# Kernel tuning notes

Measured on AMD Instinct MI355X. Metric: run time of the kernel, lower is better.

Reference implementation:

```python
import jax, jax.numpy as jnp
import numpy as np

N = 50000      # nodes
E = 800000     # edges (avg degree 16)
H = 128        # hidden_channels
L = 4          # num_layers
MAXZ = 100
EPS = 1e-5


def setup_inputs() -> dict:
    key = jax.random.key(0)
    ks = jax.random.split(key, 16)
    s = 0.05
    return {
        "z": jax.random.randint(ks[0], (N,), 0, MAXZ),
        "pos": jax.random.normal(ks[1], (N, 3), dtype=jnp.float32),
        "edge_index": jax.random.randint(ks[2], (2, E), 0, N),
        "emb": jax.random.normal(ks[3], (MAXZ, H), dtype=jnp.float32) * s,
        # edge_mlp: Linear(2H+1 -> H), SiLU, Linear(H -> H), SiLU
        "edge_w1": jax.random.normal(ks[4], (L, 2 * H + 1, H), dtype=jnp.float32) * s,
        "edge_b1": jnp.zeros((L, H), dtype=jnp.float32),
        "edge_w2": jax.random.normal(ks[5], (L, H, H), dtype=jnp.float32) * s,
        "edge_b2": jnp.zeros((L, H), dtype=jnp.float32),
        # node_mlp: Linear(2H -> H), SiLU, Linear(H -> H)
        "node_w1": jax.random.normal(ks[6], (L, 2 * H, H), dtype=jnp.float32) * s,
        "node_b1": jnp.zeros((L, H), dtype=jnp.float32),
        "node_w2": jax.random.normal(ks[7], (L, H, H), dtype=jnp.float32) * s,
        "node_b2": jnp.zeros((L, H), dtype=jnp.float32),
        "ln_g": jnp.ones((L, H), dtype=jnp.float32),
        "ln_b": jnp.zeros((L, H), dtype=jnp.float32),
    }


def _layernorm(x, g, b):
    mu = jnp.mean(x, axis=-1, keepdims=True)
    var = jnp.mean((x - mu) ** 2, axis=-1, keepdims=True)
    return g * (x - mu) / jnp.sqrt(var + EPS) + b


def reference(z, pos, edge_index, emb, edge_w1, edge_b1, edge_w2, edge_b2,
              node_w1, node_b1, node_w2, node_b2, ln_g, ln_b):
    row, col = edge_index[0], edge_index[1]
    # update_coords=False: pos is loop-invariant, so rel_pos/dist_sq computed once
    rel = pos[row] - pos[col]                       # [E, 3]
    d2 = jnp.sum(rel * rel, axis=-1, keepdims=True)  # [E, 1]
    h = emb[z]                                       # [N, H]
    n = h.shape[0]
    for l in range(L):
        edge_in = jnp.concatenate([h[row], h[col], d2], axis=-1)  # [E, 2H+1]
        m = jax.nn.silu(edge_in @ edge_w1[l] + edge_b1[l])
        m = jax.nn.silu(m @ edge_w2[l] + edge_b2[l])              # [E, H]
        agg = jax.ops.segment_sum(m, row, num_segments=n)         # [N, H]
        node_in = jnp.concatenate([h, agg], axis=-1)              # [N, 2H]
        h_new = jax.nn.silu(node_in @ node_w1[l] + node_b1[l]) @ node_w2[l] + node_b2[l]
        h = _layernorm(h + h_new, ln_g[l], ln_b[l])
    return h
```

## Files before the change

kernel.cpp:

```cpp
#include <hip/hip_runtime.h>
#include <hip/hip_bf16.h>

typedef __hip_bfloat16 hipbf16;

#define H 128
#define NLAYERS 4
#define LN_EPS 1e-5f
#define ET 64

typedef __bf16 bf16x8 __attribute__((ext_vector_type(8)));
typedef unsigned short ushort8 __attribute__((ext_vector_type(8)));
typedef float floatx16 __attribute__((ext_vector_type(16)));

union frag_u { ushort8 u; bf16x8 b; };

__device__ __forceinline__ float silu(float x) {
    return x * __builtin_amdgcn_rcpf(1.f + __expf(-x));
}
__device__ __forceinline__ float b2f_bits(unsigned short u) { return __uint_as_float(((unsigned)u) << 16); }
__device__ __forceinline__ unsigned short f2b(float f) {
    unsigned u = __float_as_uint(f);
    unsigned r = ((u >> 16) & 1u) + 0x7fffu;
    return (unsigned short)((u + r) >> 16);
}

__global__ void detect_kernel(const unsigned short* __restrict__ p, int nHalf,
                              int* __restrict__ flag) {
    int t = threadIdx.x;
    int bad = 0;
    for (int i = t; i < nHalf; i += 64) {
        unsigned short u = p[i];
        int e = (u >> 7) & 0xFF;
        if (e >= 0x8E) bad = 1;
    }
    unsigned long long m = __ballot(bad != 0);
    if (t == 0) *flag = (m != 0ULL) ? 1 : 0;
}

__global__ void conv_kernel(const void* __restrict__ src, float* __restrict__ dst,
                            int n, const int* __restrict__ flag) {
    int i = blockIdx.x * blockDim.x + threadIdx.x;
    if (i >= n) return;
    if (*flag) dst[i] = ((const float*)src)[i];
    else       dst[i] = b2f_bits(((const unsigned short*)src)[i]);
}

__global__ void pack_kernel(const float* __restrict__ W, unsigned short* __restrict__ blob,
                            int ksteps) {
    int idx = blockIdx.x * 256 + threadIdx.x;
    if (idx >= ksteps * 2048) return;
    int j  = idx & 7;
    int L  = (idx >> 3) & 63;
    int nt = (idx >> 9) & 3;
    int ks = idx >> 11;
    int k = ks * 16 + (L >> 5) * 8 + j;
    int n = nt * 32 + (L & 31);
    blob[idx] = f2b(W[k * H + n]);
}

__global__ void embed_kernel(const int* __restrict__ z, const float* __restrict__ emb,
                             float* __restrict__ h, unsigned short* __restrict__ hb, int n) {
    int idx = blockIdx.x * blockDim.x + threadIdx.x;
    if (idx >= n * H) return;
    int i = idx >> 7, j = idx & 127;
    float v = emb[z[i] * H + j];
    h[idx] = v;
    hb[idx] = f2b(v);
}

__global__ void hist_kernel(const int* __restrict__ row, int* __restrict__ cnt, int nE) {
    int i = blockIdx.x * blockDim.x + threadIdx.x;
    if (i < nE) atomicAdd(&cnt[row[i]], 1);
}

__global__ __launch_bounds__(1024) void scan_kernel(const int* __restrict__ cnt,
                                                    int* __restrict__ rptr,
                                                    int* __restrict__ cur, int nN) {
    __shared__ int wsum[17];
    __shared__ int s_carry;
    int t = threadIdx.x;
    if (t == 0) s_carry = 0;
    __syncthreads();
    for (int base = 0; base < nN; base += 1024) {
        int i = base + t;
        int v = (i < nN) ? cnt[i] : 0;
        int x = v;
        #pragma unroll
        for (int off = 1; off < 64; off <<= 1) {
            int y = __shfl_up(x, off);
            if ((t & 63) >= off) x += y;
        }
        if ((t & 63) == 63) wsum[t >> 6] = x;
        __syncthreads();
        if (t == 0) {
            int s = 0;
            #pragma unroll
            for (int w = 0; w < 16; ++w) { int tmp = wsum[w]; wsum[w] = s; s += tmp; }
            wsum[16] = s;
        }
        __syncthreads();
        int cin = s_carry;
        int excl = cin + wsum[t >> 6] + (x - v);
        if (i < nN) { rptr[i] = excl; cur[i] = excl; }
        __syncthreads();
        if (t == 0) s_carry = cin + wsum[16];
        __syncthreads();
    }
    if (t == 0) rptr[nN] = s_carry;
}

__global__ void scatter_kernel(const int* __restrict__ row, const int* __restrict__ col,
                               const float* __restrict__ pos,
                               int* __restrict__ cur,
                               int* __restrict__ rowsS, int* __restrict__ colsS,
                               float* __restrict__ d2S, int nE) {
    int e = blockIdx.x * blockDim.x + threadIdx.x;
    if (e >= nE) return;
    int r = row[e], c = col[e];
    int p = atomicAdd(&cur[r], 1);
    rowsS[p] = r;
    colsS[p] = c;
    float dx = pos[r * 3 + 0] - pos[c * 3 + 0];
    float dy = pos[r * 3 + 1] - pos[c * 3 + 1];
    float dz = pos[r * 3 + 2] - pos[c * 3 + 2];
    d2S[p] = dx * dx + dy * dy + dz * dz;
}

__global__ __launch_bounds__(256) void edge_reg(
    const unsigned short* __restrict__ hb,
    const int* __restrict__ rowsS, const int* __restrict__ colsS,
    const float* __restrict__ d2S,
    const unsigned short* __restrict__ pb1, const float* __restrict__ b1,
    const float* __restrict__ w1last,
    const unsigned short* __restrict__ pb2, const float* __restrict__ b2,
    float* __restrict__ agg, int nE)
{
    __shared__ __align__(16) unsigned short sA[ET * 264];
    __shared__ int   sRow[ET];
    __shared__ int   sCol[ET];
    __shared__ float sD2[ET];

    const int t = threadIdx.x;
    const int p0 = blockIdx.x * ET;

    if (t < ET) {
        int p = p0 + t;
        if (p < nE) { sRow[t] = rowsS[p]; sCol[t] = colsS[p]; sD2[t] = d2S[p]; }
        else        { sRow[t] = -1;       sCol[t] = 0;        sD2[t] = 0.f;    }
    }
    __syncthreads();

    #pragma unroll
    for (int i = 0; i < 8; ++i) {
        int c = t + i * 256;
        int e = c >> 5;
        int half = (c >> 4) & 1;
        int node = half ? sCol[e] : sRow[e];
        if (node < 0) node = 0;
        ushort8 v = *(const ushort8*)(hb + (size_t)node * H + (c & 15) * 8);
        *(ushort8*)(sA + e * 264 + (c & 15) * 8 + half * 128) = v;
    }
    __syncthreads();

    const int lane = t & 63;
    const int wv = t >> 6;
    const int wm = wv & 1, wn = wv >> 1;
    const int lm = lane & 31, lh = lane >> 5;
    const int n0 = wn * 64 + lm;

    const float bias10 = b1[n0], bias11 = b1[n0 + 32];
    const float wl0 = w1last[n0], wl1 = w1last[n0 + 32];
    const float bias20 = b2[n0], bias21 = b2[n0 + 32];

    floatx16 acc0 = {}, acc1 = {};
    const unsigned short* A0 = sA + (wm * 32 + lm) * 264 + lh * 8;
    #pragma unroll
    for (int ks = 0; ks < 16; ++ks) {
        frag_u a, fb0, fb1;
        a.u   = *(const ushort8*)(A0 + ks * 16);
        fb0.u = *(const ushort8*)(pb1 + (size_t)((ks * 4 + wn * 2 + 0) * 64 + lane) * 8);
        fb1.u = *(const ushort8*)(pb1 + (size_t)((ks * 4 + wn * 2 + 1) * 64 + lane) * 8);
        acc0 = __builtin_amdgcn_mfma_f32_32x32x16_bf16(a.b, fb0.b, acc0, 0, 0, 0);
        acc1 = __builtin_amdgcn_mfma_f32_32x32x16_bf16(a.b, fb1.b, acc1, 0, 0, 0);
    }
    __syncthreads();

    unsigned short* sT = sA;
    #pragma unroll
    for (int r = 0; r < 16; ++r) {
        int m = wm * 32 + (r & 3) + 8 * (r >> 2) + 4 * lh;
        float dd = sD2[m];
        sT[m * 136 + n0]      = f2b(silu(acc0[r] + bias10 + dd * wl0));
        sT[m * 136 + n0 + 32] = f2b(silu(acc1[r] + bias11 + dd * wl1));
    }
    __syncthreads();

    floatx16 c0 = {}, c1 = {};
    const unsigned short* A2 = sT + (wm * 32 + lm) * 136 + lh * 8;
    #pragma unroll
    for (int ks = 0; ks < 8; ++ks) {
        frag_u a, fb0, fb1;
        a.u   = *(const ushort8*)(A2 + ks * 16);
        fb0.u = *(const ushort8*)(pb2 + (size_t)((ks * 4 + wn * 2 + 0) * 64 + lane) * 8);
        fb1.u = *(const ushort8*)(pb2 + (size_t)((ks * 4 + wn * 2 + 1) * 64 + lane) * 8);
        c0 = __builtin_amdgcn_mfma_f32_32x32x16_bf16(a.b, fb0.b, c0, 0, 0, 0);
        c1 = __builtin_amdgcn_mfma_f32_32x32x16_bf16(a.b, fb1.b, c1, 0, 0, 0);
    }

    #pragma unroll
    for (int g = 0; g < 4; ++g) {
        const int m0 = wm * 32 + 4 * lh + 8 * g;
        int prow = sRow[m0];
        float s0 = silu(c0[g * 4] + bias20);
        float s1 = silu(c1[g * 4] + bias21);
        #pragma unroll
        for (int k = 1; k < 4; ++k) {
            int rw = sRow[m0 + k];
            float u0 = silu(c0[g * 4 + k] + bias20);
            float u1 = silu(c1[g * 4 + k] + bias21);
            if (rw == prow) {
                s0 += u0; s1 += u1;
            } else {
                if (prow >= 0) {
                    atomicAdd(&agg[(size_t)prow * H + n0],      s0);
                    atomicAdd(&agg[(size_t)prow * H + n0 + 32], s1);
                }
                prow = rw; s0 = u0; s1 = u1;
            }
        }
        if (prow >= 0) {
            atomicAdd(&agg[(size_t)prow * H + n0],      s0);
            atomicAdd(&agg[(size_t)prow * H + n0 + 32], s1);
        }
    }
}

__global__ __launch_bounds__(256) void node_mfma(
    const unsigned short* __restrict__ hb,
    const float* __restrict__ aggf,
    const unsigned short* __restrict__ pn1, const float* __restrict__ b1,
    const unsigned short* __restrict__ pn2, const float* __restrict__ b2,
    float* __restrict__ hnew, int nN)
{
    __shared__ __align__(16) unsigned short sA[ET * 264];

    const int t = threadIdx.x;
    const int i0 = blockIdx.x * ET;

    #pragma unroll
    for (int c = t; c < ET * 32; c += 256) {
        int e = c >> 5;
        int node = i0 + e; if (node >= nN) node = nN - 1;
        int f0 = (c & 31) * 8;
        ushort8 v;
        if (f0 < H) {
            v = *(const ushort8*)(hb + (size_t)node * H + f0);
        } else {
            const float* src = aggf + (size_t)node * H + (f0 - H);
            #pragma unroll
            for (int j = 0; j < 8; ++j) v[j] = f2b(src[j]);
        }
        *(ushort8*)(sA + e * 264 + (c & 31) * 8) = v;
    }
    __syncthreads();

    const int lane = t & 63;
    const int wv = t >> 6;
    const int wm = wv & 1, wn = wv >> 1;
    const int lm = lane & 31, lh = lane >> 5;
    const int n0 = wn * 64 + lm;

    floatx16 acc0 = {}, acc1 = {};
    const unsigned short* A0 = sA + (wm * 32 + lm) * 264 + lh * 8;
    #pragma unroll
    for (int ks = 0; ks < 16; ++ks) {
        frag_u a, fb0, fb1;
        a.u   = *(const ushort8*)(A0 + ks * 16);
        fb0.u = *(const ushort8*)(pn1 + (size_t)((ks * 4 + wn * 2 + 0) * 64 + lane) * 8);
        fb1.u = *(const ushort8*)(pn1 + (size_t)((ks * 4 + wn * 2 + 1) * 64 + lane) * 8);
        acc0 = __builtin_amdgcn_mfma_f32_32x32x16_bf16(a.b, fb0.b, acc0, 0, 0, 0);
        acc1 = __builtin_amdgcn_mfma_f32_32x32x16_bf16(a.b, fb1.b, acc1, 0, 0, 0);
    }
    __syncthreads();

    unsigned short* sT = sA;
    {
        float bias0 = b1[n0], bias1 = b1[n0 + 32];
        #pragma unroll
        for (int r = 0; r < 16; ++r) {
            int m = wm * 32 + (r & 3) + 8 * (r >> 2) + 4 * lh;
            sT[m * 136 + n0]      = f2b(silu(acc0[r] + bias0));
            sT[m * 136 + n0 + 32] = f2b(silu(acc1[r] + bias1));
        }
    }
    __syncthreads();

    floatx16 c0 = {}, c1 = {};
    const unsigned short* A2 = sT + (wm * 32 + lm) * 136 + lh * 8;
    #pragma unroll
    for (int ks = 0; ks < 8; ++ks) {
        frag_u a, fb0, fb1;
        a.u   = *(const ushort8*)(A2 + ks * 16);
        fb0.u = *(const ushort8*)(pn2 + (size_t)((ks * 4 + wn * 2 + 0) * 64 + lane) * 8);
        fb1.u = *(const ushort8*)(pn2 + (size_t)((ks * 4 + wn * 2 + 1) * 64 + lane) * 8);
        c0 = __builtin_amdgcn_mfma_f32_32x32x16_bf16(a.b, fb0.b, c0, 0, 0, 0);
        c1 = __builtin_amdgcn_mfma_f32_32x32x16_bf16(a.b, fb1.b, c1, 0, 0, 0);
    }
    {
        float bias0 = b2[n0], bias1 = b2[n0 + 32];
        #pragma unroll
        for (int r = 0; r < 16; ++r) {
            int m = wm * 32 + (r & 3) + 8 * (r >> 2) + 4 * lh;
            int node = i0 + m;
            if (node < nN) {
                float* dst = hnew + (size_t)node * H;
                dst[n0]      = c0[r] + bias0;
                dst[n0 + 32] = c1[r] + bias1;
            }
        }
    }
}

__global__ __launch_bounds__(256) void ln_kernel(
    float* __restrict__ h, unsigned short* __restrict__ hb,
    const float* __restrict__ hnew,
    const float* __restrict__ G, const float* __restrict__ B, int nN)
{
    __shared__ float rs[4], rq[4];
    int t = threadIdx.x;
    int local = t >> 7, j = t & 127;
    int i = blockIdx.x * 2 + local;
    float v = 0.f;
    if (i < nN) v = h[(size_t)i * H + j] + hnew[(size_t)i * H + j];
    float s = v, q = v * v;
    #pragma unroll
    for (int off = 32; off > 0; off >>= 1) {
        s += __shfl_down(s, off);
        q += __shfl_down(q, off);
    }
    int w = t >> 6;
    if ((t & 63) == 0) { rs[w] = s; rq[w] = q; }
    __syncthreads();
    int w0 = local * 2;
    float S = rs[w0] + rs[w0 + 1], Q = rq[w0] + rq[w0 + 1];
    float mu = S * (1.f / H);
    float var = Q * (1.f / H) - mu * mu;
    float y = (v - mu) * rsqrtf(var + LN_EPS) * G[j] + B[j];
    if (i < nN) {
        h[(size_t)i * H + j] = y;
        hb[(size_t)i * H + j] = f2b(y);
    }
}

__global__ void cast_kernel(const float* __restrict__ h, void* __restrict__ out,
                            int n, const int* __restrict__ flag) {
    int idx = blockIdx.x * blockDim.x + threadIdx.x;
    if (idx >= n) return;
    if (*flag) ((float*)out)[idx] = h[idx];
    else       ((hipbf16*)out)[idx] = __float2bfloat16(h[idx]);
}

extern "C" void kernel_launch(void* const* d_in, const int* in_sizes, int n_in,
                              void* d_out, int out_size, void* d_ws, size_t ws_size,
                              hipStream_t stream)
{
    const int* z  = (const int*)d_in[0];
    const int* ei = (const int*)d_in[2];

    const int nN = in_sizes[0];
    const int nE = in_sizes[2] / 2;
    const int* row = ei;
    const int* col = ei + nE;

    float* ws   = (float*)d_ws;
    int*   flag = (int*)ws;
    float* h    = ws + 64;
    unsigned short* hb = (unsigned short*)(h + (size_t)nN * H);
    float* agg  = (float*)(hb + (size_t)nN * H);
    float* conv = agg + (size_t)nN * H;

    const int n_pos = in_sizes[1];
    const int n_emb = in_sizes[3];
    const int n_ew1 = in_sizes[4], n_eb1 = in_sizes[5];
    const int n_ew2 = in_sizes[6], n_eb2 = in_sizes[7];
    const int n_nw1 = in_sizes[8], n_nb1 = in_sizes[9];
    const int n_nw2 = in_sizes[10], n_nb2 = in_sizes[11];
    const int n_lng = in_sizes[12], n_lnb = in_sizes[13];

    float* pos = conv;
    float* emb = pos + n_pos;
    float* ew1 = emb + n_emb;
    float* eb1 = ew1 + n_ew1;
    float* ew2 = eb1 + n_eb1;
    float* eb2 = ew2 + n_ew2;
    float* nw1 = eb2 + n_eb2;
    float* nb1 = nw1 + n_nw1;
    float* nw2 = nb1 + n_nb1;
    float* nb2 = nw2 + n_nw2;
    float* lng = nb2 + n_nb2;
    float* lnb = lng + n_lng;
    float* conv_end = lnb + n_lnb;

    unsigned short* pb1 = (unsigned short*)conv_end;
    unsigned short* pb2 = pb1 + 4 * 32768;
    unsigned short* pn1 = pb2 + 4 * 16384;
    unsigned short* pn2 = pn1 + 4 * 32768;

    int* cnt   = (int*)(pn2 + 4 * 16384);
    int* rptr  = cnt + nN;
    int* cur   = rptr + nN + 1;
    int* rowsS = cur + nN;
    int* colsS = rowsS + nE;
    float* d2S = (float*)(colsS + nE);

    detect_kernel<<<1, 64, 0, stream>>>((const unsigned short*)d_in[4], 4096, flag);

    struct { const void* src; float* dst; int n; } cv[12] = {
        {d_in[1],  pos, n_pos}, {d_in[3],  emb, n_emb},
        {d_in[4],  ew1, n_ew1}, {d_in[5],  eb1, n_eb1},
        {d_in[6],  ew2, n_ew2}, {d_in[7],  eb2, n_eb2},
        {d_in[8],  nw1, n_nw1}, {d_in[9],  nb1, n_nb1},
        {d_in[10], nw2, n_nw2}, {d_in[11], nb2, n_nb2},
        {d_in[12], lng, n_lng}, {d_in[13], lnb, n_lnb},
    };
    for (int i = 0; i < 12; ++i)
        conv_kernel<<<(cv[i].n + 255) / 256, 256, 0, stream>>>(cv[i].src, cv[i].dst, cv[i].n, flag);

    for (int l = 0; l < NLAYERS; ++l) {
        pack_kernel<<<128, 256, 0, stream>>>(ew1 + (size_t)l * 257 * H, pb1 + l * 32768, 16);
        pack_kernel<<<64,  256, 0, stream>>>(ew2 + (size_t)l * H * H,   pb2 + l * 16384, 8);
        pack_kernel<<<128, 256, 0, stream>>>(nw1 + (size_t)l * 2 * H * H, pn1 + l * 32768, 16);
        pack_kernel<<<64,  256, 0, stream>>>(nw2 + (size_t)l * H * H,   pn2 + l * 16384, 8);
    }

    hipMemsetAsync(cnt, 0, (size_t)nN * sizeof(int), stream);
    hist_kernel<<<(nE + 255) / 256, 256, 0, stream>>>(row, cnt, nE);
    scan_kernel<<<1, 1024, 0, stream>>>(cnt, rptr, cur, nN);
    scatter_kernel<<<(nE + 255) / 256, 256, 0, stream>>>(row, col, pos, cur, rowsS, colsS, d2S, nE);

    embed_kernel<<<(nN * H + 255) / 256, 256, 0, stream>>>(z, emb, h, hb, nN);

    const int nTiles = (nE + ET - 1) / ET;
    for (int l = 0; l < NLAYERS; ++l) {
        hipMemsetAsync(agg, 0, (size_t)nN * H * sizeof(float), stream);
        edge_reg<<<nTiles, 256, 0, stream>>>(
            hb, rowsS, colsS, d2S,
            pb1 + l * 32768, eb1 + (size_t)l * H,
            ew1 + (size_t)l * 257 * H + 256 * H,
            pb2 + l * 16384, eb2 + (size_t)l * H,
            agg, nE);
        node_mfma<<<(nN + ET - 1) / ET, 256, 0, stream>>>(
            hb, agg,
            pn1 + l * 32768, nb1 + (size_t)l * H,
            pn2 + l * 16384, nb2 + (size_t)l * H,
            agg , nN);
        ln_kernel<<<(nN + 1) / 2, 256, 0, stream>>>(
            h, hb, agg, lng + (size_t)l * H, lnb + (size_t)l * H, nN);
    }
    cast_kernel<<<(nN * H + 255) / 256, 256, 0, stream>>>(h, d_out, nN * H, flag);
}
```

Measured before the change: 1.455 ms.

## Restructure edge and node MLP kernels to per-wave 32-row tiles without block syncs

Each wavefront now owns 32 edges or nodes and all 128 output columns. It loads A fragments directly from global memory (gathered h rows, and agg converted to bf16) instead of staging through shared memory with block barriers. Per-edge metadata is exchanged via lane shuffles, and the intermediate activation goes through a per-wave shared buffer synchronized only with lgkmcnt. This removes __syncthreads and the staging pass, but doubles the per-wave accumulator registers and reads the A fragments with uncoalesced 16-byte gathers.

```diff
diff --git a/kernel.cpp b/kernel.cpp
--- a/kernel.cpp
+++ b/kernel.cpp
@@ -6,7 +6,6 @@
 #define H 128
 #define NLAYERS 4
 #define LN_EPS 1e-5f
-#define ET 64
 
 typedef __bf16 bf16x8 __attribute__((ext_vector_type(8)));
 typedef unsigned short ushort8 __attribute__((ext_vector_type(8)));
@@ -126,7 +125,7 @@
     d2S[p] = dx * dx + dy * dy + dz * dz;
 }
 
-__global__ __launch_bounds__(256) void edge_reg(
+__global__ __launch_bounds__(256, 4) void edge_wave(
     const unsigned short* __restrict__ hb,
     const int* __restrict__ rowsS, const int* __restrict__ colsS,
     const float* __restrict__ d2S,
@@ -135,187 +134,196 @@
     const unsigned short* __restrict__ pb2, const float* __restrict__ b2,
     float* __restrict__ agg, int nE)
 {
-    __shared__ __align__(16) unsigned short sA[ET * 264];
-    __shared__ int   sRow[ET];
-    __shared__ int   sCol[ET];
-    __shared__ float sD2[ET];
+    __shared__ __align__(16) unsigned short sT[4][32 * 136];
 
     const int t = threadIdx.x;
-    const int p0 = blockIdx.x * ET;
-
-    if (t < ET) {
-        int p = p0 + t;
-        if (p < nE) { sRow[t] = rowsS[p]; sCol[t] = colsS[p]; sD2[t] = d2S[p]; }
-        else        { sRow[t] = -1;       sCol[t] = 0;        sD2[t] = 0.f;    }
-    }
-    __syncthreads();
-
-    #pragma unroll
-    for (int i = 0; i < 8; ++i) {
-        int c = t + i * 256;
-        int e = c >> 5;
-        int half = (c >> 4) & 1;
-        int node = half ? sCol[e] : sRow[e];
-        if (node < 0) node = 0;
-        ushort8 v = *(const ushort8*)(hb + (size_t)node * H + (c & 15) * 8);
-        *(ushort8*)(sA + e * 264 + (c & 15) * 8 + half * 128) = v;
-    }
-    __syncthreads();
-
-    const int lane = t & 63;
-    const int wv = t >> 6;
-    const int wm = wv & 1, wn = wv >> 1;
+    const int wv = t >> 6, lane = t & 63;
     const int lm = lane & 31, lh = lane >> 5;
-    const int n0 = wn * 64 + lm;
-
-    const float bias10 = b1[n0], bias11 = b1[n0 + 32];
-    const float wl0 = w1last[n0], wl1 = w1last[n0 + 32];
-    const float bias20 = b2[n0], bias21 = b2[n0 + 32];
-
-    floatx16 acc0 = {}, acc1 = {};
-    const unsigned short* A0 = sA + (wm * 32 + lm) * 264 + lh * 8;
+    const int base = blockIdx.x * 128 + wv * 32;
+    const int p = base + lm;
+    const bool valid = p < nE;
+    const int pc = valid ? p : (nE - 1);
+
+    const int nrow = rowsS[pc];
+    const int ncol = colsS[pc];
+    const float dd = d2S[pc];
+    const int ptag = valid ? nrow : -1;
+
+    const unsigned short* rowp = hb + (size_t)nrow * H + lh * 8;
+    const unsigned short* colp = hb + (size_t)ncol * H + lh * 8;
+
+    floatx16 a0 = {}, a1 = {}, a2 = {}, a3 = {};
     #pragma unroll
     for (int ks = 0; ks < 16; ++ks) {
-        frag_u a, fb0, fb1;
-        a.u   = *(const ushort8*)(A0 + ks * 16);
-        fb0.u = *(const ushort8*)(pb1 + (size_t)((ks * 4 + wn * 2 + 0) * 64 + lane) * 8);
-        fb1.u = *(const ushort8*)(pb1 + (size_t)((ks * 4 + wn * 2 + 1) * 64 + lane) * 8);
-        acc0 = __builtin_amdgcn_mfma_f32_32x32x16_bf16(a.b, fb0.b, acc0, 0, 0, 0);
-        acc1 = __builtin_amdgcn_mfma_f32_32x32x16_bf16(a.b, fb1.b, acc1, 0, 0, 0);
-    }
-    __syncthreads();
-
-    unsigned short* sT = sA;
-    #pragma unroll
-    for (int r = 0; r < 16; ++r) {
-        int m = wm * 32 + (r & 3) + 8 * (r >> 2) + 4 * lh;
-        float dd = sD2[m];
-        sT[m * 136 + n0]      = f2b(silu(acc0[r] + bias10 + dd * wl0));
-        sT[m * 136 + n0 + 32] = f2b(silu(acc1[r] + bias11 + dd * wl1));
-    }
-    __syncthreads();
-
-    floatx16 c0 = {}, c1 = {};
-    const unsigned short* A2 = sT + (wm * 32 + lm) * 136 + lh * 8;
+        frag_u a;
+        a.u = (ks < 8) ? *(const ushort8*)(rowp + ks * 16)
+                       : *(const ushort8*)(colp + (ks - 8) * 16);
+        frag_u f0, f1, f2, f3;
+        f0.u = *(const ushort8*)(pb1 + (size_t)((ks * 4 + 0) * 64 + lane) * 8);
+        f1.u = *(const ushort8*)(pb1 + (size_t)((ks * 4 + 1) * 64 + lane) * 8);
+        f2.u = *(const ushort8*)(pb1 + (size_t)((ks * 4 + 2) * 64 + lane) * 8);
+        f3.u = *(const ushort8*)(pb1 + (size_t)((ks * 4 + 3) * 64 + lane) * 8);
+        a0 = __builtin_amdgcn_mfma_f32_32x32x16_bf16(a.b, f0.b, a0, 0, 0, 0);
+        a1 = __builtin_amdgcn_mfma_f32_32x32x16_bf16(a.b, f1.b, a1, 0, 0, 0);
+        a2 = __builtin_amdgcn_mfma_f32_32x32x16_bf16(a.b, f2.b, a2, 0, 0, 0);
+        a3 = __builtin_amdgcn_mfma_f32_32x32x16_bf16(a.b, f3.b, a3, 0, 0, 0);
+    }
+
+    unsigned short* myT = &sT[wv][0];
+    {
+        float bA0 = b1[lm], bA1 = b1[32 + lm], bA2 = b1[64 + lm], bA3 = b1[96 + lm];
+        float wA0 = w1last[lm], wA1 = w1last[32 + lm], wA2 = w1last[64 + lm], wA3 = w1last[96 + lm];
+        #pragma unroll
+        for (int r = 0; r < 16; ++r) {
+            int m = (r & 3) + 8 * (r >> 2) + 4 * lh;
+            float dm = __shfl(dd, m);
+            myT[m * 136 + lm]      = f2b(silu(a0[r] + bA0 + dm * wA0));
+            myT[m * 136 + 32 + lm] = f2b(silu(a1[r] + bA1 + dm * wA1));
+            myT[m * 136 + 64 + lm] = f2b(silu(a2[r] + bA2 + dm * wA2));
+            myT[m * 136 + 96 + lm] = f2b(silu(a3[r] + bA3 + dm * wA3));
+        }
+    }
+    __asm__ volatile("s_waitcnt lgkmcnt(0)" ::: "memory");
+
+    floatx16 c0 = {}, c1 = {}, c2 = {}, c3 = {};
+    const unsigned short* A2 = myT + lm * 136 + lh * 8;
     #pragma unroll
     for (int ks = 0; ks < 8; ++ks) {
-        frag_u a, fb0, fb1;
-        a.u   = *(const ushort8*)(A2 + ks * 16);
-        fb0.u = *(const ushort8*)(pb2 + (size_t)((ks * 4 + wn * 2 + 0) * 64 + lane) * 8);
-        fb1.u = *(const ushort8*)(pb2 + (size_t)((ks * 4 + wn * 2 + 1) * 64 + lane) * 8);
-        c0 = __builtin_amdgcn_mfma_f32_32x32x16_bf16(a.b, fb0.b, c0, 0, 0, 0);
-        c1 = __builtin_amdgcn_mfma_f32_32x32x16_bf16(a.b, fb1.b, c1, 0, 0, 0);
-    }
-
-    #pragma unroll
-    for (int g = 0; g < 4; ++g) {
-        const int m0 = wm * 32 + 4 * lh + 8 * g;
-        int prow = sRow[m0];
-        float s0 = silu(c0[g * 4] + bias20);
-        float s1 = silu(c1[g * 4] + bias21);
+        frag_u a, f0, f1, f2, f3;
+        a.u  = *(const ushort8*)(A2 + ks * 16);
+        f0.u = *(const ushort8*)(pb2 + (size_t)((ks * 4 + 0) * 64 + lane) * 8);
+        f1.u = *(const ushort8*)(pb2 + (size_t)((ks * 4 + 1) * 64 + lane) * 8);
+        f2.u = *(const ushort8*)(pb2 + (size_t)((ks * 4 + 2) * 64 + lane) * 8);
+        f3.u = *(const ushort8*)(pb2 + (size_t)((ks * 4 + 3) * 64 + lane) * 8);
+        c0 = __builtin_amdgcn_mfma_f32_32x32x16_bf16(a.b, f0.b, c0, 0, 0, 0);
+        c1 = __builtin_amdgcn_mfma_f32_32x32x16_bf16(a.b, f1.b, c1, 0, 0, 0);
+        c2 = __builtin_amdgcn_mfma_f32_32x32x16_bf16(a.b, f2.b, c2, 0, 0, 0);
+        c3 = __builtin_amdgcn_mfma_f32_32x32x16_bf16(a.b, f3.b, c3, 0, 0, 0);
+    }
+
+    {
+        float bA0 = b2[lm], bA1 = b2[32 + lm], bA2 = b2[64 + lm], bA3 = b2[96 + lm];
         #pragma unroll
-        for (int k = 1; k < 4; ++k) {
-            int rw = sRow[m0 + k];
-            float u0 = silu(c0[g * 4 + k] + bias20);
-            float u1 = silu(c1[g * 4 + k] + bias21);
-            if (rw == prow) {
-                s0 += u0; s1 += u1;
-            } else {
-                if (prow >= 0) {
-                    atomicAdd(&agg[(size_t)prow * H + n0],      s0);
-                    atomicAdd(&agg[(size_t)prow * H + n0 + 32], s1);
+        for (int g = 0; g < 4; ++g) {
+            const int m0 = 4 * lh + 8 * g;
+            int prow = __shfl(ptag, m0);
+            float s0 = silu(c0[g * 4] + bA0);
+            float s1 = silu(c1[g * 4] + bA1);
+            float s2 = silu(c2[g * 4] + bA2);
+            float s3 = silu(c3[g * 4] + bA3);
+            #pragma unroll
+            for (int k = 1; k < 4; ++k) {
+                int rw = __shfl(ptag, m0 + k);
+                float u0 = silu(c0[g * 4 + k] + bA0);
+                float u1 = silu(c1[g * 4 + k] + bA1);
+                float u2 = silu(c2[g * 4 + k] + bA2);
+                float u3 = silu(c3[g * 4 + k] + bA3);
+                if (rw == prow) {
+                    s0 += u0; s1 += u1; s2 += u2; s3 += u3;
+                } else {
+                    if (prow >= 0) {
+                        float* dst = agg + (size_t)prow * H + lm;
+                        atomicAdd(dst,      s0);
+                        atomicAdd(dst + 32, s1);
+                        atomicAdd(dst + 64, s2);
+                        atomicAdd(dst + 96, s3);
+                    }
+                    prow = rw; s0 = u0; s1 = u1; s2 = u2; s3 = u3;
                 }
-                prow = rw; s0 = u0; s1 = u1;
             }
-        }
-        if (prow >= 0) {
-            atomicAdd(&agg[(size_t)prow * H + n0],      s0);
-            atomicAdd(&agg[(size_t)prow * H + n0 + 32], s1);
-        }
-    }
-}
-
-__global__ __launch_bounds__(256) void node_mfma(
+            if (prow >= 0) {
+                float* dst = agg + (size_t)prow * H + lm;
+                atomicAdd(dst,      s0);
+                atomicAdd(dst + 32, s1);
+                atomicAdd(dst + 64, s2);
+                atomicAdd(dst + 96, s3);
+            }
+        }
+    }
+}
+
+__global__ __launch_bounds__(256, 4) void node_wave(
     const unsigned short* __restrict__ hb,
     const float* __restrict__ aggf,
     const unsigned short* __restrict__ pn1, const float* __restrict__ b1,
     const unsigned short* __restrict__ pn2, const float* __restrict__ b2,
     float* __restrict__ hnew, int nN)
 {
-    __shared__ __align__(16) unsigned short sA[ET * 264];
+    __shared__ __align__(16) unsigned short sT[4][32 * 136];
 
     const int t = threadIdx.x;
-    const int i0 = blockIdx.x * ET;
-
-    #pragma unroll
-    for (int c = t; c < ET * 32; c += 256) {
-        int e = c >> 5;
-        int node = i0 + e; if (node >= nN) node = nN - 1;
-        int f0 = (c & 31) * 8;
-        ushort8 v;
-        if (f0 < H) {
-            v = *(const ushort8*)(hb + (size_t)node * H + f0);
-        } else {
-            const float* src = aggf + (size_t)node * H + (f0 - H);
-            #pragma unroll
-            for (int j = 0; j < 8; ++j) v[j] = f2b(src[j]);
-        }
-        *(ushort8*)(sA + e * 264 + (c & 31) * 8) = v;
-    }
-    __syncthreads();
-
-    const int lane = t & 63;
-    const int wv = t >> 6;
-    const int wm = wv & 1, wn = wv >> 1;
+    const int wv = t >> 6, lane = t & 63;
     const int lm = lane & 31, lh = lane >> 5;
-    const int n0 = wn * 64 + lm;
-
-    floatx16 acc0 = {}, acc1 = {};
-    const unsigned short* A0 = sA + (wm * 32 + lm) * 264 + lh * 8;
+    const int base = blockIdx.x * 128 + wv * 32;
+    const int node = min(base + lm, nN - 1);
+
+    const unsigned short* hp = hb + (size_t)node * H + lh * 8;
+    const float* ap = aggf + (size_t)node * H + lh * 8;
+
+    floatx16 a0 = {}, a1 = {}, a2 = {}, a3 = {};
     #pragma unroll
     for (int ks = 0; ks < 16; ++ks) {
-        frag_u a, fb0, fb1;
-        a.u   = *(const ushort8*)(A0 + ks * 16);
-        fb0.u = *(const ushort8*)(pn1 + (size_t)((ks * 4 + wn * 2 + 0) * 64 + lane) * 8);
-        fb1.u = *(const ushort8*)(pn1 + (size_t)((ks * 4 + wn * 2 + 1) * 64 + lane) * 8);
-        acc0 = __builtin_amdgcn_mfma_f32_32x32x16_bf16(a.b, fb0.b, acc0, 0, 0, 0);
-        acc1 = __builtin_amdgcn_mfma_f32_32x32x16_bf16(a.b, fb1.b, acc1, 0, 0, 0);
-    }
-    __syncthreads();
-
-    unsigned short* sT = sA;
+        frag_u a;
+        if (ks < 8) {
+            a.u = *(const ushort8*)(hp + ks * 16);
+        } else {
+            float4 x = *(const float4*)(ap + (ks - 8) * 16);
+            float4 y = *(const float4*)(ap + (ks - 8) * 16 + 4);
+            a.u[0] = f2b(x.x); a.u[1] = f2b(x.y); a.u[2] = f2b(x.z); a.u[3] = f2b(x.w);
+            a.u[4] = f2b(y.x); a.u[5] = f2b(y.y); a.u[6] = f2b(y.z); a.u[7] = f2b(y.w);
+        }
+        frag_u f0, f1, f2, f3;
+        f0.u = *(const ushort8*)(pn1 + (size_t)((ks * 4 + 0) * 64 + lane) * 8);
+        f1.u = *(const ushort8*)(pn1 + (size_t)((ks * 4 + 1) * 64 + lane) * 8);
+        f2.u = *(const ushort8*)(pn1 + (size_t)((ks * 4 + 2) * 64 + lane) * 8);
+        f3.u = *(const ushort8*)(pn1 + (size_t)((ks * 4 + 3) * 64 + lane) * 8);
+        a0 = __builtin_amdgcn_mfma_f32_32x32x16_bf16(a.b, f0.b, a0, 0, 0, 0);
+        a1 = __builtin_amdgcn_mfma_f32_32x32x16_bf16(a.b, f1.b, a1, 0, 0, 0);
+        a2 = __builtin_amdgcn_mfma_f32_32x32x16_bf16(a.b, f2.b, a2, 0, 0, 0);
+        a3 = __builtin_amdgcn_mfma_f32_32x32x16_bf16(a.b, f3.b, a3, 0, 0, 0);
+    }
+
+    unsigned short* myT = &sT[wv][0];
     {
-        float bias0 = b1[n0], bias1 = b1[n0 + 32];
+        float bA0 = b1[lm], bA1 = b1[32 + lm], bA2 = b1[64 + lm], bA3 = b1[96 + lm];
         #pragma unroll
         for (int r = 0; r < 16; ++r) {
-            int m = wm * 32 + (r & 3) + 8 * (r >> 2) + 4 * lh;
-            sT[m * 136 + n0]      = f2b(silu(acc0[r] + bias0));
-            sT[m * 136 + n0 + 32] = f2b(silu(acc1[r] + bias1));
-        }
-    }
-    __syncthreads();
-
-    floatx16 c0 = {}, c1 = {};
-    const unsigned short* A2 = sT + (wm * 32 + lm) * 136 + lh * 8;
+            int m = (r & 3) + 8 * (r >> 2) + 4 * lh;
+            myT[m * 136 + lm]      = f2b(silu(a0[r] + bA0));
+            myT[m * 136 + 32 + lm] = f2b(silu(a1[r] + bA1));
+            myT[m * 136 + 64 + lm] = f2b(silu(a2[r] + bA2));
+            myT[m * 136 + 96 + lm] = f2b(silu(a3[r] + bA3));
+        }
+    }
+    __asm__ volatile("s_waitcnt lgkmcnt(0)" ::: "memory");
+
+    floatx16 c0 = {}, c1 = {}, c2 = {}, c3 = {};
+    const unsigned short* A2 = myT + lm * 136 + lh * 8;
     #pragma unroll
     for (int ks = 0; ks < 8; ++ks) {
-        frag_u a, fb0, fb1;
-        a.u   = *(const ushort8*)(A2 + ks * 16);
-        fb0.u = *(const ushort8*)(pn2 + (size_t)((ks * 4 + wn * 2 + 0) * 64 + lane) * 8);
-        fb1.u = *(const ushort8*)(pn2 + (size_t)((ks * 4 + wn * 2 + 1) * 64 + lane) * 8);
-        c0 = __builtin_amdgcn_mfma_f32_32x32x16_bf16(a.b, fb0.b, c0, 0, 0, 0);
-        c1 = __builtin_amdgcn_mfma_f32_32x32x16_bf16(a.b, fb1.b, c1, 0, 0, 0);
+        frag_u a, f0, f1, f2, f3;
+        a.u  = *(const ushort8*)(A2 + ks * 16);
+        f0.u = *(const ushort8*)(pn2 + (size_t)((ks * 4 + 0) * 64 + lane) * 8);
+        f1.u = *(const ushort8*)(pn2 + (size_t)((ks * 4 + 1) * 64 + lane) * 8);
+        f2.u = *(const ushort8*)(pn2 + (size_t)((ks * 4 + 2) * 64 + lane) * 8);
+        f3.u = *(const ushort8*)(pn2 + (size_t)((ks * 4 + 3) * 64 + lane) * 8);
+        c0 = __builtin_amdgcn_mfma_f32_32x32x16_bf16(a.b, f0.b, c0, 0, 0, 0);
+        c1 = __builtin_amdgcn_mfma_f32_32x32x16_bf16(a.b, f1.b, c1, 0, 0, 0);
+        c2 = __builtin_amdgcn_mfma_f32_32x32x16_bf16(a.b, f2.b, c2, 0, 0, 0);
+        c3 = __builtin_amdgcn_mfma_f32_32x32x16_bf16(a.b, f3.b, c3, 0, 0, 0);
     }
     {
-        float bias0 = b2[n0], bias1 = b2[n0 + 32];
+        float bA0 = b2[lm], bA1 = b2[32 + lm], bA2 = b2[64 + lm], bA3 = b2[96 + lm];
         #pragma unroll
         for (int r = 0; r < 16; ++r) {
-            int m = wm * 32 + (r & 3) + 8 * (r >> 2) + 4 * lh;
-            int node = i0 + m;
-            if (node < nN) {
-                float* dst = hnew + (size_t)node * H;
-                dst[n0]      = c0[r] + bias0;
-                dst[n0 + 32] = c1[r] + bias1;
+            int m = (r & 3) + 8 * (r >> 2) + 4 * lh;
+            int nd = base + m;
+            if (nd < nN) {
+                float* dst = hnew + (size_t)nd * H + lm;
+                dst[0]  = c0[r] + bA0;
+                dst[32] = c1[r] + bA1;
+                dst[64] = c2[r] + bA2;
+                dst[96] = c3[r] + bA3;
             }
         }
     }
@@ -440,16 +448,17 @@
 
     embed_kernel<<<(nN * H + 255) / 256, 256, 0, stream>>>(z, emb, h, hb, nN);
 
-    const int nTiles = (nE + ET - 1) / ET;
+    const int nTilesE = (nE + 127) / 128;
+    const int nTilesN = (nN + 127) / 128;
     for (int l = 0; l < NLAYERS; ++l) {
         hipMemsetAsync(agg, 0, (size_t)nN * H * sizeof(float), stream);
-        edge_reg<<<nTiles, 256, 0, stream>>>(
+        edge_wave<<<nTilesE, 256, 0, stream>>>(
             hb, rowsS, colsS, d2S,
             pb1 + l * 32768, eb1 + (size_t)l * H,
             ew1 + (size_t)l * 257 * H + 256 * H,
             pb2 + l * 16384, eb2 + (size_t)l * H,
             agg, nE);
-        node_mfma<<<(nN + ET - 1) / ET, 256, 0, stream>>>(
+        node_wave<<<nTilesN, 256, 0, stream>>>(
             hb, agg,
             pn1 + l * 32768, nb1 + (size_t)l * H,
             pn2 + l * 16384, nb2 + (size_t)l * H,
```

New measurement: 1.538 ms. 5.7% more time.
